# Optimization experiments

Measured on AMD Instinct MI355X. Metric: run time of the kernel, lower is better.

Reference implementation:

```python
import jax, jax.numpy as jnp
import numpy as np

NUM_BINS = 64


def _centers_width(num_bins):
    edges = np.linspace(-0.05, 1.05, num_bins + 1)
    delta = edges[2] - edges[1]
    centers = (edges + delta / 2)[:-1]
    return jnp.asarray(centers, jnp.float32), jnp.float32(delta / 2)

_CENTERS, _WIDTH = _centers_width(NUM_BINS)

_YUV = jnp.asarray([[0.299, 0.587, 0.114],
                    [-0.14713, -0.28886, 0.436],
                    [0.615, -0.51499, -0.10001]], jnp.float32)


def _soft_hist(img):
    # img: [B, C, H, W]; scale from [-1,1] -> [0,1] as in extract_hist
    img = (img + 1.0) * 0.5
    # bin_centers_conv (w=1, b=-center) -> x - c ; abs ; bin_widths_conv (w=-1, b=width) -> width - |x-c|
    d = jnp.abs(img[:, :, None, :, :] - _CENTERS[None, None, :, None, None])  # [B,C,bins,H,W]
    act = jnp.float32(1.01) ** (_WIDTH - d)
    act = jnp.where(act > 1.0, act, 0.0)  # nn.Threshold(1, 0)
    return act.mean(axis=(3, 4))  # AdaptiveAvgPool2d(1) -> [B, C, bins]


def _to_yuv(x):
    return jnp.einsum('ij,bjhw->bihw', _YUV, x)


def _emd(h1, h2):
    # per channel: mean over batch of sum over bins of cumsum diff; summed over channels
    diff = jnp.cumsum(h1, axis=-1) - jnp.cumsum(h2, axis=-1)  # [B,C,bins]
    return diff.sum(axis=-1).mean(axis=0).sum()


def setup_inputs() -> dict:
    key = jax.random.key(0)
    k1, k2 = jax.random.split(key)
    shape = (8, 3, 256, 256)
    return {
        'input_img': jax.random.normal(k1, shape, dtype=jnp.float32),
        'reference_img': jax.random.normal(k2, shape, dtype=jnp.float32),
    }


def reference(input_img, reference_img):
    total = _emd(_soft_hist(input_img), _soft_hist(reference_img))  # rgb
    total = total + _emd(_soft_hist(_to_yuv(input_img)), _soft_hist(_to_yuv(reference_img)))  # yuv
    return total
```

## Files before the change

kernel.cpp:

```cpp
#include <hip/hip_runtime.h>


#define HW    65536
#define NPIX  524288
#define BLOCK 256
#define PXT   2
#define NBLK  (NPIX / (BLOCK * PXT))

__device__ __forceinline__ void contrib(double v, float vf,
    const float* __restrict__ centers, double width, float ga, float gb, float Lf,
    int& aW, float& aE) {
  float gg = fmaf(vf, ga, gb);
  int k0 = (int)floorf(gg);
  double u = (v + 1.0) * 0.5;
  #pragma unroll
  for (int dk = 0; dk <= 1; ++dk) {
    int k = k0 + dk;
    if ((unsigned)k < 64u) {
      double d = u - (double)centers[k];
      double t = width - fabs(d);
      if (t > 0.0) {
        float tf = (float)t;
        float z  = Lf * tf;
        float e  = fmaf(0.5f * z, z, z);
        int   w  = 64 - k;
        aW += w;
        aE  = fmaf((float)w, e, aE);
      }
    }
  }
}

__global__ __launch_bounds__(BLOCK) void hl_partial(
    const float* __restrict__ img_in, const float* __restrict__ img_ref,
    double* __restrict__ partials) {
  __shared__ float centers[64];
  __shared__ double redW[4], redE[4];

  const double start = -0.05;
  const double step  = (1.05 - (-0.05)) / 64.0;
  const double e1    = 1.0 * step + start;
  const double e2    = 2.0 * step + start;
  const double halfw = (e2 - e1) * 0.5;
  const float  widthf = (float)halfw;
  if (threadIdx.x < 64) {
    double edge = (double)(int)threadIdx.x * step + start;
    centers[threadIdx.x] = (float)(edge + halfw);
  }
  __syncthreads();

  const double width = (double)widthf;
  const float  Lf = (float)log((double)1.01f);
  const float  ga = (float)(0.5 / step);
  const float  gb = (float)(0.55 / step - 0.5);

  const double Y0 = (double)0.299f,    Y1 = (double)0.587f,    Y2 = (double)0.114f;
  const double U0 = (double)-0.14713f, U1 = (double)-0.28886f, U2 = (double)0.436f;
  const double V0 = (double)0.615f,    V1 = (double)-0.51499f, V2 = (double)-0.10001f;

  int   aWp = 0,  aWn = 0;
  float aEp = 0.f, aEn = 0.f;

  const int base = blockIdx.x * (BLOCK * PXT) + threadIdx.x;
  #pragma unroll
  for (int i = 0; i < PXT; ++i) {
    int p  = base + i * BLOCK;
    int b  = p >> 16;
    int hw = p & (HW - 1);
    const float* pi = img_in  + (size_t)b * (3 * HW) + hw;
    const float* pr = img_ref + (size_t)b * (3 * HW) + hw;
    float r0 = pi[0], g0 = pi[HW], b0 = pi[2 * HW];
    float r1 = pr[0], g1 = pr[HW], b1 = pr[2 * HW];

    contrib((double)r0, r0, centers, width, ga, gb, Lf, aWp, aEp);
    contrib((double)g0, g0, centers, width, ga, gb, Lf, aWp, aEp);
    contrib((double)b0, b0, centers, width, ga, gb, Lf, aWp, aEp);
    contrib((double)r1, r1, centers, width, ga, gb, Lf, aWn, aEn);
    contrib((double)g1, g1, centers, width, ga, gb, Lf, aWn, aEn);
    contrib((double)b1, b1, centers, width, ga, gb, Lf, aWn, aEn);

    double yi = fma(Y2, (double)b0, fma(Y1, (double)g0, Y0 * (double)r0));
    double ui = fma(U2, (double)b0, fma(U1, (double)g0, U0 * (double)r0));
    double vi = fma(V2, (double)b0, fma(V1, (double)g0, V0 * (double)r0));
    double yr = fma(Y2, (double)b1, fma(Y1, (double)g1, Y0 * (double)r1));
    double ur = fma(U2, (double)b1, fma(U1, (double)g1, U0 * (double)r1));
    double vr = fma(V2, (double)b1, fma(V1, (double)g1, V0 * (double)r1));

    contrib(yi, (float)yi, centers, width, ga, gb, Lf, aWp, aEp);
    contrib(ui, (float)ui, centers, width, ga, gb, Lf, aWp, aEp);
    contrib(vi, (float)vi, centers, width, ga, gb, Lf, aWp, aEp);
    contrib(yr, (float)yr, centers, width, ga, gb, Lf, aWn, aEn);
    contrib(ur, (float)ur, centers, width, ga, gb, Lf, aWn, aEn);
    contrib(vr, (float)vr, centers, width, ga, gb, Lf, aWn, aEn);
  }

  int    aW = aWp - aWn;
  double aE = (double)aEp - (double)aEn;

  #pragma unroll
  for (int off = 32; off > 0; off >>= 1) {
    aW += __shfl_down(aW, off);
    aE += __shfl_down(aE, off);
  }
  int wv = threadIdx.x >> 6;
  if ((threadIdx.x & 63) == 0) { redW[wv] = (double)aW; redE[wv] = aE; }
  __syncthreads();

  if (threadIdx.x == 0) {
    double sW = 0.0, sE = 0.0;
    #pragma unroll
    for (int w = 0; w < 4; ++w) { sW += redW[w]; sE += redE[w]; }
    partials[2 * blockIdx.x]     = sW;
    partials[2 * blockIdx.x + 1] = sE;
  }
}

__global__ __launch_bounds__(BLOCK) void hl_final(
    const double* __restrict__ partials, float* __restrict__ out) {
  __shared__ double redW[4], redE[4];
  double sW = 0.0, sE = 0.0;
  for (int b = threadIdx.x; b < NBLK; b += BLOCK) {
    sW += partials[2 * b];
    sE += partials[2 * b + 1];
  }
  #pragma unroll
  for (int off = 32; off > 0; off >>= 1) {
    sW += __shfl_down(sW, off);
    sE += __shfl_down(sE, off);
  }
  int wv = threadIdx.x >> 6;
  if ((threadIdx.x & 63) == 0) { redW[wv] = sW; redE[wv] = sE; }
  __syncthreads();
  if (threadIdx.x == 0) {
    double tW = 0.0, tE = 0.0;
    #pragma unroll
    for (int w = 0; w < 4; ++w) { tW += redW[w]; tE += redE[w]; }
    out[0] = (float)((tW + tE) * (1.0 / (double)NPIX));
  }
}

extern "C" void kernel_launch(void* const* d_in, const int* in_sizes, int n_in,
                              void* d_out, int out_size, void* d_ws, size_t ws_size,
                              hipStream_t stream) {
  const float* img_in  = (const float*)d_in[0];
  const float* img_ref = (const float*)d_in[1];
  float* out = (float*)d_out;
  double* partials = (double*)d_ws;

  hl_partial<<<NBLK, BLOCK, 0, stream>>>(img_in, img_ref, partials);
  hl_final<<<1, BLOCK, 0, stream>>>(partials, out);
}
```

Measured before the change: 71.12 us.

## Replace double-precision bin lookup with branchless float math and float2 loads

Computes the two candidate bin contributions per value with branchless single-precision arithmetic based on the fractional bin position, instead of double-precision distance to centers read from shared memory. The centers table and its syncthreads are removed, the YUV conversion moves to float, and each thread loads two adjacent pixels per channel with float2 vector loads. This is meant to cut the slow FP64 work and the divergent branches; the risk is small numerical drift from float rounding near bin edges, and float accumulation of the integer weights.

```diff
diff --git a/kernel.cpp b/kernel.cpp
--- a/kernel.cpp
+++ b/kernel.cpp
@@ -7,94 +7,85 @@
 #define PXT   2
 #define NBLK  (NPIX / (BLOCK * PXT))
 
-__device__ __forceinline__ void contrib(double v, float vf,
-    const float* __restrict__ centers, double width, float ga, float gb, float Lf,
-    int& aW, float& aE) {
-  float gg = fmaf(vf, ga, gb);
-  int k0 = (int)floorf(gg);
-  double u = (v + 1.0) * 0.5;
-  #pragma unroll
-  for (int dk = 0; dk <= 1; ++dk) {
-    int k = k0 + dk;
-    if ((unsigned)k < 64u) {
-      double d = u - (double)centers[k];
-      double t = width - fabs(d);
-      if (t > 0.0) {
-        float tf = (float)t;
-        float z  = Lf * tf;
-        float e  = fmaf(0.5f * z, z, z);
-        int   w  = 64 - k;
-        aW += w;
-        aE  = fmaf((float)w, e, aE);
-      }
-    }
-  }
+__device__ __forceinline__ void contrib(float v, float ivs, float go, float Ls,
+                                        float& aW, float& aE) {
+  float u  = (v + 1.0f) * 0.5f;
+  float g  = fmaf(u, ivs, go);
+  float kf = floorf(g);
+  float f  = g - kf;
+  float t0 = 0.5f - f;
+  float t1 = f - 0.5f;
+  bool in0 = (t0 > 0.0f) && (fabsf(kf - 31.5f) < 32.5f);
+  bool in1 = (t1 > 0.0f) && (fabsf(kf - 30.5f) < 32.5f);
+  float w0 = in0 ? (64.0f - kf) : 0.0f;
+  float w1 = in1 ? (63.0f - kf) : 0.0f;
+  float z0 = t0 * Ls;
+  float z1 = t1 * Ls;
+  float e0 = fmaf(0.5f * z0, z0, z0);
+  float e1 = fmaf(0.5f * z1, z1, z1);
+  aW += w0 + w1;
+  aE  = fmaf(w0, e0, aE);
+  aE  = fmaf(w1, e1, aE);
 }
 
 __global__ __launch_bounds__(BLOCK) void hl_partial(
     const float* __restrict__ img_in, const float* __restrict__ img_ref,
     double* __restrict__ partials) {
-  __shared__ float centers[64];
   __shared__ double redW[4], redE[4];
 
   const double start = -0.05;
   const double step  = (1.05 - (-0.05)) / 64.0;
-  const double e1    = 1.0 * step + start;
-  const double e2    = 2.0 * step + start;
-  const double halfw = (e2 - e1) * 0.5;
-  const float  widthf = (float)halfw;
-  if (threadIdx.x < 64) {
-    double edge = (double)(int)threadIdx.x * step + start;
-    centers[threadIdx.x] = (float)(edge + halfw);
-  }
-  __syncthreads();
+  const float  ivs = (float)(1.0 / step);
+  const float  go  = (float)(0.05 / step - 0.5);
+  const float  Ls  = (float)(log((double)1.01f) * step);
 
-  const double width = (double)widthf;
-  const float  Lf = (float)log((double)1.01f);
-  const float  ga = (float)(0.5 / step);
-  const float  gb = (float)(0.55 / step - 0.5);
+  const float Y0 = 0.299f,    Y1 = 0.587f,    Y2 = 0.114f;
+  const float U0 = -0.14713f, U1 = -0.28886f, U2 = 0.436f;
+  const float V0 = 0.615f,    V1 = -0.51499f, V2 = -0.10001f;
 
-  const double Y0 = (double)0.299f,    Y1 = (double)0.587f,    Y2 = (double)0.114f;
-  const double U0 = (double)-0.14713f, U1 = (double)-0.28886f, U2 = (double)0.436f;
-  const double V0 = (double)0.615f,    V1 = (double)-0.51499f, V2 = (double)-0.10001f;
-
-  int   aWp = 0,  aWn = 0;
+  float aWp = 0.f, aWn = 0.f;
   float aEp = 0.f, aEn = 0.f;
 
-  const int base = blockIdx.x * (BLOCK * PXT) + threadIdx.x;
+  const int pair = blockIdx.x * BLOCK + threadIdx.x;
+  const int p    = pair << 1;
+  const int b    = p >> 16;
+  const int hw   = p & (HW - 1);
+  const float2* pi = (const float2*)(img_in  + (size_t)b * (3 * HW) + hw);
+  const float2* pr = (const float2*)(img_ref + (size_t)b * (3 * HW) + hw);
+  float2 r0 = pi[0], g0 = pi[HW / 2], b0 = pi[HW];
+  float2 r1 = pr[0], g1 = pr[HW / 2], b1 = pr[HW];
+
+  const float rr0[2] = { r0.x, r0.y }, gg0[2] = { g0.x, g0.y }, bb0[2] = { b0.x, b0.y };
+  const float rr1[2] = { r1.x, r1.y }, gg1[2] = { g1.x, g1.y }, bb1[2] = { b1.x, b1.y };
+
   #pragma unroll
   for (int i = 0; i < PXT; ++i) {
-    int p  = base + i * BLOCK;
-    int b  = p >> 16;
-    int hw = p & (HW - 1);
-    const float* pi = img_in  + (size_t)b * (3 * HW) + hw;
-    const float* pr = img_ref + (size_t)b * (3 * HW) + hw;
-    float r0 = pi[0], g0 = pi[HW], b0 = pi[2 * HW];
-    float r1 = pr[0], g1 = pr[HW], b1 = pr[2 * HW];
+    float ri = rr0[i], gi = gg0[i], bi = bb0[i];
+    float rj = rr1[i], gj = gg1[i], bj = bb1[i];
 
-    contrib((double)r0, r0, centers, width, ga, gb, Lf, aWp, aEp);
-    contrib((double)g0, g0, centers, width, ga, gb, Lf, aWp, aEp);
-    contrib((double)b0, b0, centers, width, ga, gb, Lf, aWp, aEp);
-    contrib((double)r1, r1, centers, width, ga, gb, Lf, aWn, aEn);
-    contrib((double)g1, g1, centers, width, ga, gb, Lf, aWn, aEn);
-    contrib((double)b1, b1, centers, width, ga, gb, Lf, aWn, aEn);
+    contrib(ri, ivs, go, Ls, aWp, aEp);
+    contrib(gi, ivs, go, Ls, aWp, aEp);
+    contrib(bi, ivs, go, Ls, aWp, aEp);
+    contrib(rj, ivs, go, Ls, aWn, aEn);
+    contrib(gj, ivs, go, Ls, aWn, aEn);
+    contrib(bj, ivs, go, Ls, aWn, aEn);
 
-    double yi = fma(Y2, (double)b0, fma(Y1, (double)g0, Y0 * (double)r0));
-    double ui = fma(U2, (double)b0, fma(U1, (double)g0, U0 * (double)r0));
-    double vi = fma(V2, (double)b0, fma(V1, (double)g0, V0 * (double)r0));
-    double yr = fma(Y2, (double)b1, fma(Y1, (double)g1, Y0 * (double)r1));
-    double ur = fma(U2, (double)b1, fma(U1, (double)g1, U0 * (double)r1));
-    double vr = fma(V2, (double)b1, fma(V1, (double)g1, V0 * (double)r1));
+    float yi = fmaf(Y2, bi, fmaf(Y1, gi, Y0 * ri));
+    float ui = fmaf(U2, bi, fmaf(U1, gi, U0 * ri));
+    float vi = fmaf(V2, bi, fmaf(V1, gi, V0 * ri));
+    float yj = fmaf(Y2, bj, fmaf(Y1, gj, Y0 * rj));
+    float uj = fmaf(U2, bj, fmaf(U1, gj, U0 * rj));
+    float vj = fmaf(V2, bj, fmaf(V1, gj, V0 * rj));
 
-    contrib(yi, (float)yi, centers, width, ga, gb, Lf, aWp, aEp);
-    contrib(ui, (float)ui, centers, width, ga, gb, Lf, aWp, aEp);
-    contrib(vi, (float)vi, centers, width, ga, gb, Lf, aWp, aEp);
-    contrib(yr, (float)yr, centers, width, ga, gb, Lf, aWn, aEn);
-    contrib(ur, (float)ur, centers, width, ga, gb, Lf, aWn, aEn);
-    contrib(vr, (float)vr, centers, width, ga, gb, Lf, aWn, aEn);
+    contrib(yi, ivs, go, Ls, aWp, aEp);
+    contrib(ui, ivs, go, Ls, aWp, aEp);
+    contrib(vi, ivs, go, Ls, aWp, aEp);
+    contrib(yj, ivs, go, Ls, aWn, aEn);
+    contrib(uj, ivs, go, Ls, aWn, aEn);
+    contrib(vj, ivs, go, Ls, aWn, aEn);
   }
 
-  int    aW = aWp - aWn;
+  float  aW = aWp - aWn;
   double aE = (double)aEp - (double)aEn;
 
   #pragma unroll
```

New measurement: 66.21 us. 6.9% less time.
